# Kernel optimization log

Hardware: AMD Instinct MI355X
Metric: run time of the kernel (lower is better)

Reference implementation:

```python
import jax, jax.numpy as jnp
import numpy as np

NUM_HEADS = 8
NUM_Q = 64
RANK = 64
DIM = 768
LN_EPS = 1e-5


def setup_inputs() -> dict:
    key = jax.random.key(0)
    ks = jax.random.split(key, 8)
    b, n = 4, 1024
    x = jax.random.normal(ks[0], (b, NUM_Q, DIM), dtype=jnp.float32)
    context = jax.random.normal(ks[1], (b, n, DIM), dtype=jnp.float32)
    s = 0.02
    Wq = jax.random.normal(ks[2], (DIM, DIM), dtype=jnp.float32) * s
    Wk = jax.random.normal(ks[3], (DIM, DIM), dtype=jnp.float32) * s
    Wv1 = jax.random.normal(ks[4], (DIM, NUM_Q * RANK), dtype=jnp.float32) * s
    ln_g = jnp.ones((NUM_Q * RANK,), dtype=jnp.float32)
    ln_b = jnp.zeros((NUM_Q * RANK,), dtype=jnp.float32)
    Wc = jax.random.normal(ks[5], (NUM_Q, RANK, DIM), dtype=jnp.float32) * s
    Wout = jax.random.normal(ks[6], (DIM, DIM), dtype=jnp.float32) * s
    return {"x": x, "context": context, "Wq": Wq, "Wk": Wk, "Wv1": Wv1,
            "ln_g": ln_g, "ln_b": ln_b, "Wc": Wc, "Wout": Wout}


def reference(x, context, Wq, Wk, Wv1, ln_g, ln_b, Wc, Wout):
    b, nq, d = x.shape
    n = context.shape[1]
    h, dh = NUM_HEADS, d // NUM_HEADS

    q = x @ Wq                      # [b, nq, d]
    k = context @ Wk                # [b, n, d]

    # q-aware V: Linear -> LayerNorm(all_q_mid) -> grouped 1x1 conv (per-query rank->d)
    h1 = context @ Wv1              # [b, n, NUM_Q*RANK]
    mu = jnp.mean(h1, axis=-1, keepdims=True)
    var = jnp.var(h1, axis=-1, keepdims=True)
    h1 = (h1 - mu) * jax.lax.rsqrt(var + LN_EPS) * ln_g + ln_b
    vmid = h1.reshape(b, n, NUM_Q, RANK)
    v = jnp.einsum('bnqr,qrd->bqnd', vmid, Wc)   # [b, NUM_Q, n, d]
    # split heads: 'b q n (h dh) -> b h q n dh'
    v = v.reshape(b, NUM_Q, n, h, dh).transpose(0, 3, 1, 2, 4)

    qh = q.reshape(b, nq, h, dh).transpose(0, 2, 1, 3)   # [b,h,nq,dh]
    kh = k.reshape(b, n, h, dh).transpose(0, 2, 1, 3)    # [b,h,n,dh]
    scale = dh ** (-0.25)
    sim = jnp.einsum('bhid,bhjd->bhij', qh * scale, kh * scale)
    attn = jax.nn.softmax(sim, axis=-1)                  # [b,h,nq,n]
    out = jnp.einsum('bhij,bhijd->bhid', attn, v)        # per-query V
    out = out.transpose(0, 2, 1, 3).reshape(b, nq, d)
    return out @ Wout
```

## Files before the change

### kernel.cpp

```cpp
#include <hip/hip_runtime.h>
#include <math.h>

typedef unsigned short ushort_t;
typedef __bf16 bf16x8 __attribute__((ext_vector_type(8)));
typedef float f32x4 __attribute__((ext_vector_type(4)));

__device__ __forceinline__ ushort_t f2b_rne(float f) {
    union { float f; unsigned int u; } c;
    c.f = f;
    unsigned int u = c.u;
    u += 0x7FFFu + ((u >> 16) & 1u);
    return (ushort_t)(u >> 16);
}
__device__ __forceinline__ float b2f(ushort_t v) {
    union { unsigned int u; float f; } c;
    c.u = ((unsigned int)v) << 16;
    return c.f;
}

__device__ __forceinline__ void gl_lds16(const ushort_t* g, ushort_t* l) {
    __builtin_amdgcn_global_load_lds(
        (const __attribute__((address_space(1))) void*)g,
        (__attribute__((address_space(3))) void*)l, 16, 0, 0);
}

__global__ __launch_bounds__(256) void prep(
    const float* __restrict__ x, const float* __restrict__ context,
    const float* __restrict__ Wq, const float* __restrict__ Wk,
    const float* __restrict__ Wv1, const float* __restrict__ Wout,
    ushort_t* __restrict__ x_b, ushort_t* __restrict__ ctx_b,
    ushort_t* __restrict__ Wq_t, ushort_t* __restrict__ Wk_t,
    ushort_t* __restrict__ Wv1_t, ushort_t* __restrict__ Wout_b,
    float* __restrict__ colzero,
    int b, int n) {
    const int t = threadIdx.x;
    const int bid = blockIdx.x;
    const int nb_x = (b * 64 * 768 / 4) / 256;
    const int nb_c = (b * n * 768 / 4) / 256;

    if (bid < nb_x + nb_c) {
        const float* in = (bid < nb_x) ? x : context;
        ushort_t* outp = (bid < nb_x) ? x_b : ctx_b;
        const int i = ((bid < nb_x) ? bid : (bid - nb_x)) * 256 + t;
        float4 v = ((const float4*)in)[i];
        ushort_t o[4] = {f2b_rne(v.x), f2b_rne(v.y), f2b_rne(v.z), f2b_rne(v.w)};
        *(uint2*)&outp[(size_t)i * 4] = *(uint2*)o;
        return;
    }

    int u = bid - nb_x - nb_c;
    if (u >= 4800) {
        const int idx = (u - 4800) * 256 + t;
        ((float4*)colzero)[idx] = make_float4(0.f, 0.f, 0.f, 0.f);
        return;
    }
    if (u >= 4224) {
        const int i = (u - 4224) * 256 + t;
        float4 v = ((const float4*)Wout)[i];
        ushort_t o[4] = {f2b_rne(v.x), f2b_rne(v.y), f2b_rne(v.z), f2b_rne(v.w)};
        *(uint2*)&Wout_b[(size_t)i * 4] = *(uint2*)o;
        return;
    }

    const float* in;
    ushort_t* outp;
    int R = 768, C = 768;
    if (u < 576)        { in = Wq;  outp = Wq_t; }
    else if (u < 1152)  { u -= 576;  in = Wk;  outp = Wk_t; }
    else                { u -= 1152; in = Wv1; outp = Wv1_t; C = 4096; }
    const int ct = C / 32;
    const int c0 = (u % ct) * 32, r0 = (u / ct) * 32;
    const int tx = t & 31, ty = t >> 5;

    __shared__ float tt[32][33];
#pragma unroll
    for (int i = 0; i < 4; i++)
        tt[ty + 8 * i][tx] = in[(size_t)(r0 + ty + 8 * i) * C + c0 + tx];
    __syncthreads();
#pragma unroll
    for (int i = 0; i < 4; i++)
        outp[(size_t)(c0 + ty + 8 * i) * R + r0 + tx] = f2b_rne(tt[tx][ty + 8 * i]);
}

__global__ __launch_bounds__(256) void gemm3(
    const ushort_t* __restrict__ x_b, const ushort_t* __restrict__ ctx_b,
    const ushort_t* __restrict__ Wq_t, const ushort_t* __restrict__ Wk_t,
    const ushort_t* __restrict__ Wv1_t,
    ushort_t* __restrict__ qb, ushort_t* __restrict__ kb,
    ushort_t* __restrict__ h1t, int b, int n) {
    const int bid = blockIdx.x;
    const int tq = (b * 64 / 128) * 6;
    const int tk = (b * n / 128) * 6;
    const int Mn = b * n;

    const ushort_t *A, *Bt;
    ushort_t* C;
    int N, row0, col0;
    if (bid < tq) {
        A = x_b; Bt = Wq_t; C = qb; N = 768;
        row0 = (bid / 6) * 128; col0 = (bid % 6) * 128;
    } else if (bid < tq + tk) {
        const int u = bid - tq;
        A = ctx_b; Bt = Wk_t; C = kb; N = 768;
        row0 = (u / 6) * 128; col0 = (u % 6) * 128;
    } else {
        const int u = bid - tq - tk;
        A = Wv1_t; Bt = ctx_b; C = h1t; N = Mn;
        row0 = (u % 32) * 128; col0 = (u / 32) * 128;
    }
    const int K = 768;

    __shared__ ushort_t As[2 * 128 * 32];
    __shared__ ushort_t Bs[2 * 128 * 32];

    const int t = threadIdx.x;
    const int lane = t & 63;
    const int wave = t >> 6;
    const int quad = lane >> 4;
    const int l15 = lane & 15;
    const int wm = (wave >> 1) * 64;
    const int wn = (wave & 1) * 64;

    const ushort_t* gA0 = A + (size_t)(row0 + (t >> 2)) * K + (t & 3) * 8;
    const ushort_t* gA1 = gA0 + (size_t)64 * K;
    const ushort_t* gB0 = Bt + (size_t)(col0 + (t >> 2)) * K + (t & 3) * 8;
    const ushort_t* gB1 = gB0 + (size_t)64 * K;

    ushort_t* lA0 = &As[wave * 512];
    ushort_t* lA1 = &As[2048 + wave * 512];
    ushort_t* lA2 = &As[4096 + wave * 512];
    ushort_t* lA3 = &As[6144 + wave * 512];
    ushort_t* lB0 = &Bs[wave * 512];
    ushort_t* lB1 = &Bs[2048 + wave * 512];
    ushort_t* lB2 = &Bs[4096 + wave * 512];
    ushort_t* lB3 = &Bs[6144 + wave * 512];

    f32x4 acc[4][4] = {};

    for (int k0 = 0; k0 < K; k0 += 64) {
        __syncthreads();
        gl_lds16(gA0 + k0, lA0);
        gl_lds16(gA1 + k0, lA1);
        gl_lds16(gA0 + k0 + 32, lA2);
        gl_lds16(gA1 + k0 + 32, lA3);
        gl_lds16(gB0 + k0, lB0);
        gl_lds16(gB1 + k0, lB1);
        gl_lds16(gB0 + k0 + 32, lB2);
        gl_lds16(gB1 + k0 + 32, lB3);
        __syncthreads();

#pragma unroll
        for (int ks = 0; ks < 2; ks++) {
            bf16x8 af[4], bfr[4];
#pragma unroll
            for (int i = 0; i < 4; i++)
                af[i] = *(const bf16x8*)&As[ks * 4096 + (wm + i * 16 + l15) * 32 + quad * 8];
#pragma unroll
            for (int j = 0; j < 4; j++)
                bfr[j] = *(const bf16x8*)&Bs[ks * 4096 + (wn + j * 16 + l15) * 32 + quad * 8];
#pragma unroll
            for (int i = 0; i < 4; i++)
#pragma unroll
                for (int j = 0; j < 4; j++)
                    acc[i][j] = __builtin_amdgcn_mfma_f32_16x16x32_bf16(
                        af[i], bfr[j], acc[i][j], 0, 0, 0);
        }
    }

#pragma unroll
    for (int i = 0; i < 4; i++)
#pragma unroll
        for (int j = 0; j < 4; j++)
#pragma unroll
            for (int r = 0; r < 4; r++) {
                const int row = row0 + wm + i * 16 + quad * 4 + r;
                const int col = col0 + wn + j * 16 + l15;
                C[(size_t)row * N + col] = f2b_rne(acc[i][j][r]);
            }
}

__global__ __launch_bounds__(256) void scores_stats(
    const ushort_t* __restrict__ qb, const ushort_t* __restrict__ kb,
    const ushort_t* __restrict__ h1t, float* __restrict__ S,
    float* __restrict__ colsum, float* __restrict__ colsumsq,
    int b, int n, int Mn) {
    __shared__ ushort_t sb[192 * 104];
    const int t = threadIdx.x;
    const int nsc = b * 8 * (n / 128);

    if (blockIdx.x >= nsc) {
        const int u = blockIdx.x - nsc;
        const int rc = u >> 4;
        const int cc = u & 15;
        const int cg = t & 31;
        const int rg = t >> 5;
        const ushort_t* p =
            h1t + (size_t)(rc * 256 + rg * 32) * Mn + cc * 256 + cg * 8;
        float s[8] = {}, s2[8] = {};
#pragma unroll 4
        for (int r = 0; r < 32; r++) {
            const bf16x8 v = *(const bf16x8*)&p[(size_t)r * Mn];
#pragma unroll
            for (int j = 0; j < 8; j++) {
                const float f = (float)v[j];
                s[j] += f;
                s2[j] += f * f;
            }
        }
        float* red = (float*)sb;
#pragma unroll
        for (int j = 0; j < 8; j++) {
            red[rg * 256 + cg * 8 + j] = s[j];
            red[2048 + rg * 256 + cg * 8 + j] = s2[j];
        }
        __syncthreads();
        float ts = 0.f, ts2 = 0.f;
#pragma unroll
        for (int g = 0; g < 8; g++) {
            ts += red[g * 256 + t];
            ts2 += red[2048 + g * 256 + t];
        }
        atomicAdd(&colsum[cc * 256 + t], ts);
        atomicAdd(&colsumsq[cc * 256 + t], ts2);
        return;
    }

    const int nt = n / 128;
    const int n0 = (blockIdx.x % nt) * 128;
    const int bh = blockIdx.x / nt;
    const int bb = bh >> 3, h = bh & 7;
    const int lane = t & 63, wave = t >> 6;
    const int quad = lane >> 4, l15 = lane & 15;
    const int wm = (wave >> 1) * 32;
    const int wn = (wave & 1) * 64;

    ushort_t* Qs = sb;
    ushort_t* Ks = sb + 64 * 104;

    for (int g = t; g < 768; g += 256) {
        const int r = g / 12, s = g - r * 12;
        *(bf16x8*)&Qs[r * 104 + s * 8] =
            *(const bf16x8*)&qb[(size_t)(bb * 64 + r) * 768 + h * 96 + s * 8];
    }
    for (int g = t; g < 1536; g += 256) {
        const int r = g / 12, s = g - r * 12;
        *(bf16x8*)&Ks[r * 104 + s * 8] =
            *(const bf16x8*)&kb[(size_t)(bb * n + n0 + r) * 768 + h * 96 + s * 8];
    }
    __syncthreads();

    f32x4 acc[2][4] = {};
#pragma unroll
    for (int ks = 0; ks < 3; ks++) {
        bf16x8 af[2], bfr[4];
#pragma unroll
        for (int i = 0; i < 2; i++)
            af[i] = *(const bf16x8*)&Qs[(wm + i * 16 + l15) * 104 + ks * 32 + quad * 8];
#pragma unroll
        for (int j = 0; j < 4; j++)
            bfr[j] = *(const bf16x8*)&Ks[(wn + j * 16 + l15) * 104 + ks * 32 + quad * 8];
#pragma unroll
        for (int i = 0; i < 2; i++)
#pragma unroll
            for (int j = 0; j < 4; j++)
                acc[i][j] = __builtin_amdgcn_mfma_f32_16x16x32_bf16(
                    af[i], bfr[j], acc[i][j], 0, 0, 0);
    }

    const float sc = 0.10206207261596575f;
    float* Sp = S + (size_t)bh * 64 * n;
#pragma unroll
    for (int i = 0; i < 2; i++)
#pragma unroll
        for (int j = 0; j < 4; j++)
#pragma unroll
            for (int r = 0; r < 4; r++) {
                const int row = wm + i * 16 + quad * 4 + r;
                const int col = n0 + wn + j * 16 + l15;
                Sp[(size_t)row * n + col] = acc[i][j][r] * sc;
            }
}

__global__ __launch_bounds__(1024) void attn_fused(
    const float* __restrict__ S, const float* __restrict__ colsum,
    const float* __restrict__ colsumsq, const ushort_t* __restrict__ h1t,
    const float* __restrict__ ln_g, const float* __restrict__ ln_b,
    const float* __restrict__ Wc, const ushort_t* __restrict__ Wout_b,
    float* __restrict__ out, int n, int Mn) {
    const int bq = blockIdx.x;
    const int bb = bq >> 6, qi = bq & 63;
    const int tid = threadIdx.x;
    const int lane = tid & 63, wv = tid >> 6;
    const int quad = lane >> 4, l15 = lane & 15;

    __shared__ ushort_t sW[9 * 1032];
    __shared__ ushort_t sH[64 * 264];
    __shared__ float sl[8], swmu[8];
    __shared__ float pm[16], pl[16], pwm[16];
    __shared__ float sA[512];
    __shared__ float sO[768];

    float* sMu = (float*)sH;
    float* sRs = (float*)sH + 1024;

    for (int i = tid; i < n; i += 1024) {
        const float cs = colsum[bb * n + i];
        const float cq = colsumsq[bb * n + i];
        const float m = cs * (1.0f / 4096.0f);
        sMu[i] = m;
        sRs[i] = rsqrtf(cq * (1.0f / 4096.0f) - m * m + 1e-5f);
    }
    for (int i = tid; i < 1032; i += 1024) sW[8 * 1032 + i] = 0;
    __syncthreads();

    const int h = wv >> 1;
    const int half = wv & 1;
    const int nh = n >> 1;
    const int i0 = half * nh;
    const float* Sp = S + ((size_t)(bb * 8 + h) * 64 + qi) * n;
    {
        float m = -1e30f;
        for (int i = i0 + lane; i < i0 + nh; i += 64) m = fmaxf(m, Sp[i]);
#pragma unroll
        for (int off = 32; off > 0; off >>= 1) m = fmaxf(m, __shfl_down(m, off));
        if (lane == 0) pm[wv] = m;
    }
    __syncthreads();
    const float mh = fmaxf(pm[2 * h], pm[2 * h + 1]);
    {
        float l = 0.f, wm = 0.f;
        for (int i = i0 + lane; i < i0 + nh; i += 64) {
            const float e = expf(Sp[i] - mh);
            const float w = e * sRs[i];
            const ushort_t wb = f2b_rne(w);
            sW[h * 1032 + i] = wb;
            l += e;
            wm += b2f(wb) * sMu[i];
        }
#pragma unroll
        for (int off = 32; off > 0; off >>= 1) {
            l += __shfl_down(l, off);
            wm += __shfl_down(wm, off);
        }
        if (lane == 0) { pl[wv] = l; pwm[wv] = wm; }
    }
    __syncthreads();
    if (tid < 8) {
        sl[tid] = pl[2 * tid] + pl[2 * tid + 1];
        swmu[tid] = pwm[2 * tid] + pwm[2 * tid + 1];
    }

    const int mrow = (l15 < 8 ? l15 : 8) * 1032;
    f32x4 acc = {};
    const int nch = n >> 8;
    for (int ch = 0; ch < nch; ch++) {
        __syncthreads();
        for (int g = tid; g < 2048; g += 1024) {
            const int row = g >> 5, seg = g & 31;
            *(bf16x8*)&sH[row * 264 + seg * 8] =
                *(const bf16x8*)&h1t[(size_t)(qi * 64 + row) * Mn + bb * n +
                                     ch * 256 + seg * 8];
        }
        __syncthreads();
        if (wv < 4) {
#pragma unroll
            for (int ks = 0; ks < 8; ks++) {
                const bf16x8 af = *(const bf16x8*)&sW[mrow + ch * 256 + ks * 32 + quad * 8];
                const bf16x8 bf = *(const bf16x8*)&sH[(wv * 16 + l15) * 264 + ks * 32 + quad * 8];
                acc = __builtin_amdgcn_mfma_f32_16x16x32_bf16(af, bf, acc, 0, 0, 0);
            }
        }
    }
    __syncthreads();

    if (wv < 4) {
#pragma unroll
        for (int r = 0; r < 4; r++) {
            const int hh = quad * 4 + r;
            if (hh < 8) {
                const int rr = wv * 16 + l15;
                const int c = qi * 64 + rr;
                sA[hh * 64 + rr] =
                    ln_g[c] * ((acc[r] - swmu[hh]) / sl[hh]) + ln_b[c];
            }
        }
    }
    __syncthreads();

    for (int d = tid; d < 768; d += 1024) {
        const int hh = d / 96;
        const float* wp = Wc + (size_t)qi * 49152 + d;
        float a = 0.f;
#pragma unroll
        for (int r = 0; r < 64; r++) a += sA[hh * 64 + r] * wp[(size_t)r * 768];
        sO[d] = b2f(f2b_rne(a));
    }
    __syncthreads();

    if (tid < 768) {
        const int dout = tid;
        const float4* sO4 = (const float4*)sO;
        float a0 = 0.f, a1 = 0.f, a2 = 0.f, a3 = 0.f;
#pragma unroll 4
        for (int d4 = 0; d4 < 192; d4++) {
            const float4 s4 = sO4[d4];
            const int d = d4 * 4;
            a0 += s4.x * b2f(Wout_b[(size_t)d * 768 + dout]);
            a1 += s4.y * b2f(Wout_b[(size_t)(d + 1) * 768 + dout]);
            a2 += s4.z * b2f(Wout_b[(size_t)(d + 2) * 768 + dout]);
            a3 += s4.w * b2f(Wout_b[(size_t)(d + 3) * 768 + dout]);
        }
        out[(size_t)bq * 768 + dout] = (a0 + a1) + (a2 + a3);
    }
}

extern "C" void kernel_launch(void* const* d_in, const int* in_sizes, int n_in,
                              void* d_out, int out_size, void* d_ws, size_t ws_size,
                              hipStream_t stream) {
    const float* x       = (const float*)d_in[0];
    const float* context = (const float*)d_in[1];
    const float* Wq      = (const float*)d_in[2];
    const float* Wk      = (const float*)d_in[3];
    const float* Wv1     = (const float*)d_in[4];
    const float* ln_g    = (const float*)d_in[5];
    const float* ln_b    = (const float*)d_in[6];
    const float* Wc      = (const float*)d_in[7];
    const float* Wout    = (const float*)d_in[8];
    float* out = (float*)d_out;

    const int b = in_sizes[0] / (64 * 768);
    const int n = in_sizes[1] / (b * 768);
    const int M  = b * 64;
    const int Mn = b * n;

    float* ws = (float*)d_ws;
    size_t off = 0;
    float* S       = ws + off;  off += (size_t)b * 8 * 64 * n;
    float* colsum  = ws + off;  off += (size_t)Mn;
    float* colsumsq= ws + off;  off += (size_t)Mn;

    ushort_t* us = (ushort_t*)(ws + off);
    size_t uo = 0;
    ushort_t* x_b    = us + uo;  uo += (size_t)M * 768;
    ushort_t* ctx_b  = us + uo;  uo += (size_t)Mn * 768;
    ushort_t* qb     = us + uo;  uo += (size_t)M * 768;
    ushort_t* kb     = us + uo;  uo += (size_t)Mn * 768;
    ushort_t* h1t    = us + uo;  uo += (size_t)Mn * 4096;
    ushort_t* Wq_t   = us + uo;  uo += (size_t)768 * 768;
    ushort_t* Wk_t   = us + uo;  uo += (size_t)768 * 768;
    ushort_t* Wv1_t  = us + uo;  uo += (size_t)4096 * 768;
    ushort_t* Wout_b = us + uo;  uo += (size_t)768 * 768;

    const int nb_x = (M * 768 / 4) / 256;
    const int nb_c = (Mn * 768 / 4) / 256;
    prep<<<nb_x + nb_c + 4800 + 8, 256, 0, stream>>>(
        x, context, Wq, Wk, Wv1, Wout, x_b, ctx_b, Wq_t, Wk_t, Wv1_t, Wout_b,
        colsum, b, n);

    const int tq = (M / 128) * 6, tk = (Mn / 128) * 6;
    const int th = (4096 / 128) * (Mn / 128);
    gemm3<<<tq + tk + th, 256, 0, stream>>>(x_b, ctx_b, Wq_t, Wk_t, Wv1_t,
                                            qb, kb, h1t, b, n);

    scores_stats<<<b * 8 * (n / 128) + 256, 256, 0, stream>>>(
        qb, kb, h1t, S, colsum, colsumsq, b, n, Mn);

    attn_fused<<<M, 1024, 0, stream>>>(S, colsum, colsumsq, h1t, ln_g, ln_b,
                                       Wc, Wout_b, out, n, Mn);
}
```

Measured before the change: 178.6 us.

## Split attention kernel across head pairs with atomic output accumulation

Result: slower. 199.7 us (+11.8%).

```diff
diff --git a/kernel.cpp b/kernel.cpp
--- a/kernel.cpp
+++ b/kernel.cpp
@@ -32,6 +32,7 @@
     ushort_t* __restrict__ Wq_t, ushort_t* __restrict__ Wk_t,
     ushort_t* __restrict__ Wv1_t, ushort_t* __restrict__ Wout_b,
     float* __restrict__ colzero,
+    float* __restrict__ outz,
     int b, int n) {
     const int t = threadIdx.x;
     const int bid = blockIdx.x;
@@ -49,6 +50,11 @@
     }
 
     int u = bid - nb_x - nb_c;
+    if (u >= 4808) {
+        const int idx = (u - 4808) * 256 + t;
+        ((float4*)outz)[idx] = make_float4(0.f, 0.f, 0.f, 0.f);
+        return;
+    }
     if (u >= 4800) {
         const int idx = (u - 4800) * 256 + t;
         ((float4*)colzero)[idx] = make_float4(0.f, 0.f, 0.f, 0.f);
@@ -281,59 +287,62 @@
             }
 }
 
-__global__ __launch_bounds__(1024) void attn_fused(
+__global__ __launch_bounds__(512) void attn_split(
     const float* __restrict__ S, const float* __restrict__ colsum,
     const float* __restrict__ colsumsq, const ushort_t* __restrict__ h1t,
     const float* __restrict__ ln_g, const float* __restrict__ ln_b,
     const float* __restrict__ Wc, const ushort_t* __restrict__ Wout_b,
     float* __restrict__ out, int n, int Mn) {
-    const int bq = blockIdx.x;
+    const int a = blockIdx.x;
+    const int bq = blockIdx.y;
     const int bb = bq >> 6, qi = bq & 63;
     const int tid = threadIdx.x;
     const int lane = tid & 63, wv = tid >> 6;
     const int quad = lane >> 4, l15 = lane & 15;
-
-    __shared__ ushort_t sW[9 * 1032];
+    const int h0 = a * 2;
+
+    __shared__ ushort_t sW[3 * 1032];
     __shared__ ushort_t sH[64 * 264];
-    __shared__ float sl[8], swmu[8];
-    __shared__ float pm[16], pl[16], pwm[16];
-    __shared__ float sA[512];
-    __shared__ float sO[768];
+    __shared__ float pm[8], pl[8], pwm[8];
+    __shared__ float sl[2], swmu[2];
+    __shared__ float sA[2 * 64];
+    __shared__ float sO[192];
 
     float* sMu = (float*)sH;
     float* sRs = (float*)sH + 1024;
 
-    for (int i = tid; i < n; i += 1024) {
+    for (int i = tid; i < n; i += 512) {
         const float cs = colsum[bb * n + i];
         const float cq = colsumsq[bb * n + i];
         const float m = cs * (1.0f / 4096.0f);
         sMu[i] = m;
         sRs[i] = rsqrtf(cq * (1.0f / 4096.0f) - m * m + 1e-5f);
     }
-    for (int i = tid; i < 1032; i += 1024) sW[8 * 1032 + i] = 0;
-    __syncthreads();
-
-    const int h = wv >> 1;
-    const int half = wv & 1;
-    const int nh = n >> 1;
-    const int i0 = half * nh;
-    const float* Sp = S + ((size_t)(bb * 8 + h) * 64 + qi) * n;
+    for (int i = tid; i < 1032; i += 512) sW[2 * 1032 + i] = 0;
+    __syncthreads();
+
+    const int hl = wv >> 2;
+    const int qt = wv & 3;
+    const int nq4 = n >> 2;
+    const int i0 = qt * nq4;
+    const float* Sp = S + ((size_t)(bb * 8 + h0 + hl) * 64 + qi) * n;
     {
         float m = -1e30f;
-        for (int i = i0 + lane; i < i0 + nh; i += 64) m = fmaxf(m, Sp[i]);
+        for (int i = i0 + lane; i < i0 + nq4; i += 64) m = fmaxf(m, Sp[i]);
 #pragma unroll
         for (int off = 32; off > 0; off >>= 1) m = fmaxf(m, __shfl_down(m, off));
         if (lane == 0) pm[wv] = m;
     }
     __syncthreads();
-    const float mh = fmaxf(pm[2 * h], pm[2 * h + 1]);
+    const float mh = fmaxf(fmaxf(pm[hl * 4], pm[hl * 4 + 1]),
+                           fmaxf(pm[hl * 4 + 2], pm[hl * 4 + 3]));
     {
         float l = 0.f, wm = 0.f;
-        for (int i = i0 + lane; i < i0 + nh; i += 64) {
+        for (int i = i0 + lane; i < i0 + nq4; i += 64) {
             const float e = expf(Sp[i] - mh);
             const float w = e * sRs[i];
             const ushort_t wb = f2b_rne(w);
-            sW[h * 1032 + i] = wb;
+            sW[hl * 1032 + i] = wb;
             l += e;
             wm += b2f(wb) * sMu[i];
         }
@@ -345,17 +354,17 @@
         if (lane == 0) { pl[wv] = l; pwm[wv] = wm; }
     }
     __syncthreads();
-    if (tid < 8) {
-        sl[tid] = pl[2 * tid] + pl[2 * tid + 1];
-        swmu[tid] = pwm[2 * tid] + pwm[2 * tid + 1];
-    }
-
-    const int mrow = (l15 < 8 ? l15 : 8) * 1032;
+    if (tid < 2) {
+        sl[tid] = pl[tid * 4] + pl[tid * 4 + 1] + pl[tid * 4 + 2] + pl[tid * 4 + 3];
+        swmu[tid] = pwm[tid * 4] + pwm[tid * 4 + 1] + pwm[tid * 4 + 2] + pwm[tid * 4 + 3];
+    }
+
+    const int mrow = (l15 < 2 ? l15 : 2) * 1032;
     f32x4 acc = {};
     const int nch = n >> 8;
     for (int ch = 0; ch < nch; ch++) {
         __syncthreads();
-        for (int g = tid; g < 2048; g += 1024) {
+        for (int g = tid; g < 2048; g += 512) {
             const int row = g >> 5, seg = g & 31;
             *(bf16x8*)&sH[row * 264 + seg * 8] =
                 *(const bf16x8*)&h1t[(size_t)(qi * 64 + row) * Mn + bb * n +
@@ -373,44 +382,40 @@
     }
     __syncthreads();
 
-    if (wv < 4) {
-#pragma unroll
-        for (int r = 0; r < 4; r++) {
-            const int hh = quad * 4 + r;
-            if (hh < 8) {
-                const int rr = wv * 16 + l15;
-                const int c = qi * 64 + rr;
-                sA[hh * 64 + rr] =
-                    ln_g[c] * ((acc[r] - swmu[hh]) / sl[hh]) + ln_b[c];
-            }
-        }
-    }
-    __syncthreads();
-
-    for (int d = tid; d < 768; d += 1024) {
-        const int hh = d / 96;
-        const float* wp = Wc + (size_t)qi * 49152 + d;
-        float a = 0.f;
-#pragma unroll
-        for (int r = 0; r < 64; r++) a += sA[hh * 64 + r] * wp[(size_t)r * 768];
-        sO[d] = b2f(f2b_rne(a));
-    }
-    __syncthreads();
-
-    if (tid < 768) {
-        const int dout = tid;
+    if (wv < 4 && quad == 0) {
+#pragma unroll
+        for (int r = 0; r < 2; r++) {
+            const int rr = wv * 16 + l15;
+            const int c = qi * 64 + rr;
+            sA[r * 64 + rr] = ln_g[c] * ((acc[r] - swmu[r]) / sl[r]) + ln_b[c];
+        }
+    }
+    __syncthreads();
+
+    if (tid < 192) {
+        const int dg = a * 192 + tid;
+        const int hl2 = tid / 96;
+        const float* wp = Wc + (size_t)qi * 49152 + dg;
+        float acc2 = 0.f;
+#pragma unroll
+        for (int r = 0; r < 64; r++) acc2 += sA[hl2 * 64 + r] * wp[(size_t)r * 768];
+        sO[tid] = b2f(f2b_rne(acc2));
+    }
+    __syncthreads();
+
+    for (int dout = tid; dout < 768; dout += 512) {
         const float4* sO4 = (const float4*)sO;
         float a0 = 0.f, a1 = 0.f, a2 = 0.f, a3 = 0.f;
 #pragma unroll 4
-        for (int d4 = 0; d4 < 192; d4++) {
+        for (int d4 = 0; d4 < 48; d4++) {
             const float4 s4 = sO4[d4];
-            const int d = d4 * 4;
+            const int d = a * 192 + d4 * 4;
             a0 += s4.x * b2f(Wout_b[(size_t)d * 768 + dout]);
             a1 += s4.y * b2f(Wout_b[(size_t)(d + 1) * 768 + dout]);
             a2 += s4.z * b2f(Wout_b[(size_t)(d + 2) * 768 + dout]);
             a3 += s4.w * b2f(Wout_b[(size_t)(d + 3) * 768 + dout]);
         }
-        out[(size_t)bq * 768 + dout] = (a0 + a1) + (a2 + a3);
+        atomicAdd(&out[(size_t)bq * 768 + dout], (a0 + a1) + (a2 + a3));
     }
 }
 
@@ -453,9 +458,10 @@
 
     const int nb_x = (M * 768 / 4) / 256;
     const int nb_c = (Mn * 768 / 4) / 256;
-    prep<<<nb_x + nb_c + 4800 + 8, 256, 0, stream>>>(
+    const int nb_oz = (M * 768 / 4) / 256;
+    prep<<<nb_x + nb_c + 4800 + 8 + nb_oz, 256, 0, stream>>>(
         x, context, Wq, Wk, Wv1, Wout, x_b, ctx_b, Wq_t, Wk_t, Wv1_t, Wout_b,
-        colsum, b, n);
+        colsum, out, b, n);
 
     const int tq = (M / 128) * 6, tk = (Mn / 128) * 6;
     const int th = (4096 / 128) * (Mn / 128);
@@ -465,6 +471,6 @@
     scores_stats<<<b * 8 * (n / 128) + 256, 256, 0, stream>>>(
         qb, kb, h1t, S, colsum, colsumsq, b, n, Mn);
 
-    attn_fused<<<M, 1024, 0, stream>>>(S, colsum, colsumsq, h1t, ln_g, ln_b,
-                                       Wc, Wout_b, out, n, Mn);
-}
+    attn_split<<<dim3(4, M), 512, 0, stream>>>(S, colsum, colsumsq, h1t,
+                                               ln_g, ln_b, Wc, Wout_b, out, n, Mn);
+}
```
